# Performance work log

Measured on AMD Instinct MI355X. Metric: run time of the kernel, lower is better.

Reference implementation:

```python
import jax, jax.numpy as jnp
import numpy as np

NP, P, NS = 5, 5, 15  # body parts, joints per part, segments per scale


def _gauss_forward(x):
    # x: (batch, nb_frames, joints=NP*P, coordinates, 1)
    b, T, J, C, _ = x.shape
    inp = x.reshape(b, T, NP, P, C, 1)
    # lengths of the 6 temporal windows: full, two halves, three thirds
    seg_lens = [T, T // 2, T - T // 2, T // 3, T // 3, T - 2 * (T // 3)]
    outs = []
    for L in seg_lens:
        nb_fr = L // NS
        # first NS-1 segments of nb_fr frames each, always starting at frame 0
        head = inp[:, :(NS - 1) * nb_fr].reshape(b, NS - 1, nb_fr, NP, P, C, 1)
        mu_h = head.mean(axis=2)                    # (b, NS-1, NP, P, C, 1)
        xc = head - mu_h[:, :, None]
        cov_h = jnp.einsum('bkfnpci,bkfnpdi->bknpcd', xc, xc) / nb_fr
        # last segment runs to the END of the full sequence (faithful to original)
        tail = inp[:, (NS - 1) * nb_fr:]
        rest = tail.shape[1]
        mu_t = tail.mean(axis=1)                    # (b, NP, P, C, 1)
        xt = tail - mu_t[:, None]
        cov_t = jnp.einsum('bfnpci,bfnpdi->bnpcd', xt, xt) / rest
        mu = jnp.concatenate([mu_h, mu_t[:, None]], axis=1)    # (b, NS, NP, P, C, 1)
        cov = jnp.concatenate([cov_h, cov_t[:, None]], axis=1)  # (b, NS, NP, P, C, C)
        # match torch layout (b, NP, NS, P, ...)
        mu = jnp.transpose(mu, (0, 2, 1, 3, 4, 5))
        cov = jnp.transpose(cov, (0, 2, 1, 3, 4, 5))
        muT = jnp.swapaxes(mu, -1, -2)
        elt00 = cov + mu @ muT                       # E[xx^T]
        ones = jnp.ones(mu.shape[:-2] + (1, 1), dtype=x.dtype)
        top = jnp.concatenate([elt00, mu], axis=-1)
        bot = jnp.concatenate([muT, ones], axis=-1)
        outs.append(jnp.concatenate([top, bot], axis=-2))
    # (b, 6, NP, NS, P, C+1, C+1)
    return jnp.stack(outs, axis=1)


def setup_inputs() -> dict:
    key = jax.random.key(0)
    x = jax.random.normal(key, (256, 2048, 25, 3, 1), dtype=jnp.float32)
    return {"x": x}


def reference(x):
    return _gauss_forward(x)
```

## Files before the change

### kernel.cpp

```cpp
#include <hip/hip_runtime.h>
#include <stdint.h>


#define NSEG_MAX 40
#define IDXPK 0x9210287517640543ull

struct Tab {
    int n;
    uint32_t p[NSEG_MAX];
    uint32_t cr[45];
};

__global__ __launch_bounds__(256) void p1_kernel(const float* __restrict__ x,
                                                 float* __restrict__ ws, Tab tab) {
    __shared__ float lds[2250];
    int pc = blockIdx.x, b = blockIdx.y;
    uint32_t pk = tab.p[pc];
    int f0 = pk & 0xffff, L = (int)(pk >> 16);
    int tid = threadIdx.x;

    float s0=0.f,s1=0.f,s2=0.f,s3=0.f,s4=0.f,s5=0.f,s6=0.f,s7=0.f,s8=0.f;
    if (tid < 250) {
        int fslot = tid / 25;
        const float* q = x + (size_t)b * 153600 + (size_t)f0 * 75 + tid * 3;
        int nk = (L - fslot + 9) / 10;
        #pragma unroll 3
        for (int k = 0; k < nk; ++k, q += 750) {
            float a = q[0], bb = q[1], c = q[2];
            s0 += a;      s1 += bb;     s2 += c;
            s3 += a * a;  s4 += a * bb; s5 += a * c;
            s6 += bb * bb; s7 += bb * c; s8 += c * c;
        }
        float* l = &lds[tid * 9];
        l[0]=s0; l[1]=s1; l[2]=s2; l[3]=s3; l[4]=s4; l[5]=s5; l[6]=s6; l[7]=s7; l[8]=s8;
    }
    __syncthreads();
    if (tid < 225) {
        float v = 0.f;
        #pragma unroll
        for (int fs = 0; fs < 10; ++fs) v += lds[fs * 225 + tid];
        ws[((size_t)b * tab.n + pc) * 225 + tid] = v;
    }
}

__global__ __launch_bounds__(256) void p2_kernel(const float* __restrict__ ws,
                                                 float* __restrict__ out, Tab tab) {
    __shared__ float sws[1620];
    __shared__ float red[2032];
    __shared__ float invn[45];
    int b = blockIdx.x, np = blockIdx.y;
    int tid = threadIdx.x;
    int n = tab.n;
    int tot = n * 45;
    const float* wb = ws + (size_t)b * n * 225 + np * 45;
    for (int i = tid; i < tot; i += 256) {
        int piece = i / 45, idx = i - piece * 45;
        sws[i] = wb[(size_t)piece * 225 + idx];
    }
    if (tid < 45) {
        int st = tid / 15, ch = tid - st * 15;
        const int nst[3] = {136, 68, 45};
        int ns = nst[st];
        int nfr = (ch == 14) ? (2048 - 14 * ns) : ns;
        invn[tid] = 1.0f / (float)nfr;
    }
    __syncthreads();

    for (int i = tid; i < 2025; i += 256) {
        int sc = i / 45, idx = i - sc * 45;
        uint32_t r = tab.cr[sc];
        int p0 = (int)(r & 0xffff), p1 = (int)(r >> 16);
        float v = 0.f;
        for (int p = p0; p < p1; ++p) v += sws[p * 45 + idx];
        red[i] = v;
    }
    __syncthreads();

    float4* ob4 = (float4*)(out + (size_t)b * 36000 + (size_t)np * 1200);
    for (int q = tid; q < 1800; q += 256) {
        int seg = q / 300;
        int q2  = q - seg * 300;
        int ch  = q2 / 20;
        int rem = q2 - ch * 20;
        int p   = rem >> 2;
        int r   = rem & 3;
        int st  = (seg == 0) ? 0 : (seg < 3) ? 1 : 2;
        int sc  = st * 15 + ch;
        float inv = invn[sc];
        const float* rb = &red[sc * 45 + p * 9];
        uint64_t pkk = IDXPK >> (16 * r);
        float4 v;
        v.x = rb[(int)(pkk & 15)] * inv;
        v.y = rb[(int)((pkk >> 4) & 15)] * inv;
        v.z = rb[(int)((pkk >> 8) & 15)] * inv;
        v.w = (r == 3) ? 1.0f : rb[(int)((pkk >> 12) & 15)] * inv;
        ob4[(size_t)seg * 1500 + q2] = v;
    }
}

__global__ __launch_bounds__(256) void gauss_fallback(const float* __restrict__ x,
                                                      float* __restrict__ out) {
    __shared__ float lds[2250];
    __shared__ float red[225];
    __shared__ float outm[400];
    int bid = blockIdx.x;
    int chunk = bid % 15;
    int tmp = bid / 15;
    int stype = tmp % 3;
    int b = tmp / 3;
    const int nbs[3] = {136, 68, 45};
    int ns = nbs[stype];
    int f0 = chunk * ns;
    int f1 = (chunk == 14) ? 2048 : (f0 + ns);
    float inv_n = 1.0f / (float)(f1 - f0);
    int tid = threadIdx.x;
    if (tid < 250) {
        int j = tid % 25, tsub = tid / 25;
        const float* base = x + (size_t)b * 153600 + j * 3;
        float s0=0.f,s1=0.f,s2=0.f,s3=0.f,s4=0.f,s5=0.f,s6=0.f,s7=0.f,s8=0.f;
        for (int t = f0 + tsub; t < f1; t += 10) {
            const float* p = base + (size_t)t * 75;
            float x0 = p[0], x1 = p[1], x2 = p[2];
            s0+=x0; s1+=x1; s2+=x2;
            s3+=x0*x0; s4+=x0*x1; s5+=x0*x2;
            s6+=x1*x1; s7+=x1*x2; s8+=x2*x2;
        }
        float* l = &lds[tid * 9];
        l[0]=s0; l[1]=s1; l[2]=s2; l[3]=s3; l[4]=s4; l[5]=s5; l[6]=s6; l[7]=s7; l[8]=s8;
    }
    __syncthreads();
    if (tid < 225) {
        float v = 0.f;
        #pragma unroll
        for (int ts = 0; ts < 10; ++ts) v += lds[ts * 225 + tid];
        red[tid] = v;
    }
    __syncthreads();
    if (tid < 25) {
        const float* r = &red[tid * 9];
        float mu0=r[0]*inv_n, mu1=r[1]*inv_n, mu2=r[2]*inv_n;
        float m00=r[3]*inv_n, m01=r[4]*inv_n, m02=r[5]*inv_n;
        float m11=r[6]*inv_n, m12=r[7]*inv_n, m22=r[8]*inv_n;
        float* o = &outm[tid * 16];
        o[0]=m00; o[1]=m01; o[2]=m02; o[3]=mu0;
        o[4]=m01; o[5]=m11; o[6]=m12; o[7]=mu1;
        o[8]=m02; o[9]=m12; o[10]=m22; o[11]=mu2;
        o[12]=mu0; o[13]=mu1; o[14]=mu2; o[15]=1.0f;
    }
    __syncthreads();
    int so0 = (stype == 0) ? 0 : (stype == 1) ? 1 : 3;
    int ndup = (stype == 0) ? 1 : (stype == 1) ? 2 : 3;
    int total = 400 * ndup;
    size_t obase = (size_t)b * 36000 + (size_t)chunk * 80;
    for (int idx = tid; idx < total; idx += 256) {
        int dup = idx / 400;
        int r = idx % 400;
        int np = r / 80;
        int rem = r % 80;
        out[obase + (size_t)(so0 + dup) * 6000 + (size_t)np * 1200 + rem] = outm[r];
    }
}

static void build_tab(Tab& tab) {
    unsigned char isb[2049];
    for (int i = 0; i <= 2048; ++i) isb[i] = 0;
    isb[2048] = 1;
    for (int k = 1; k <= 14; ++k) { isb[45 * k] = 1; isb[68 * k] = 1; isb[136 * k] = 1; }
    int n = 0, prev = 0;
    int pf0[NSEG_MAX];
    for (int f = 1; f <= 2048; ++f) {
        if (!isb[f]) continue;
        pf0[n] = prev;
        tab.p[n++] = (uint32_t)(prev | ((f - prev) << 16));
        prev = f;
    }
    tab.n = n;
    const int nst[3] = {136, 68, 45};
    for (int st = 0; st < 3; ++st) {
        int ns = nst[st];
        for (int c = 0; c < 15; ++c) {
            int a = c * ns, bnd = (c == 14) ? 2048 : (c + 1) * ns;
            int p0 = 0; while (p0 < n && pf0[p0] < a) ++p0;
            int p1 = p0; while (p1 < n && pf0[p1] < bnd) ++p1;
            tab.cr[st * 15 + c] = (uint32_t)(p0 | (p1 << 16));
        }
    }
}

extern "C" void kernel_launch(void* const* d_in, const int* in_sizes, int n_in,
                              void* d_out, int out_size, void* d_ws, size_t ws_size,
                              hipStream_t stream) {
    const float* x = (const float*)d_in[0];
    float* out = (float*)d_out;
    Tab tab;
    build_tab(tab);
    size_t need = (size_t)256 * tab.n * 225 * sizeof(float);

    if (ws_size >= need) {
        float* ws = (float*)d_ws;
        dim3 g1(tab.n, 256);
        p1_kernel<<<g1, 256, 0, stream>>>(x, ws, tab);
        dim3 g2(256, 5);
        p2_kernel<<<g2, 256, 0, stream>>>(ws, out, tab);
    } else {
        gauss_fallback<<<256 * 45, 256, 0, stream>>>(x, out);
    }
}
```

Before: 239.5 us.

## Fuse piece reduction and output assembly into one kernel via last-block counter

Merges the two kernels into one. Each block writes its partial sums, then bumps a per-batch atomic counter, and the last block to finish for a batch performs the second-stage reduction and output writes for all five body parts. This removes the second kernel launch and the gap between kernels, but needs a memset for the counters and serialises the tail work of each batch into a single block. The first loop's unroll factor also goes from 3 to 5.

```diff
diff --git a/kernel.cpp b/kernel.cpp
--- a/kernel.cpp
+++ b/kernel.cpp
@@ -11,52 +11,54 @@
     uint32_t cr[45];
 };
 
-__global__ __launch_bounds__(256) void p1_kernel(const float* __restrict__ x,
-                                                 float* __restrict__ ws, Tab tab) {
-    __shared__ float lds[2250];
+__global__ __launch_bounds__(256) void fused_kernel(const float* __restrict__ x,
+                                                    float* __restrict__ ws,
+                                                    unsigned* __restrict__ cnt,
+                                                    float* __restrict__ out, Tab tab) {
+    __shared__ float smem[3870];
+    __shared__ int lastFlag;
     int pc = blockIdx.x, b = blockIdx.y;
+    int n = tab.n;
     uint32_t pk = tab.p[pc];
     int f0 = pk & 0xffff, L = (int)(pk >> 16);
     int tid = threadIdx.x;
 
-    float s0=0.f,s1=0.f,s2=0.f,s3=0.f,s4=0.f,s5=0.f,s6=0.f,s7=0.f,s8=0.f;
     if (tid < 250) {
         int fslot = tid / 25;
         const float* q = x + (size_t)b * 153600 + (size_t)f0 * 75 + tid * 3;
         int nk = (L - fslot + 9) / 10;
-        #pragma unroll 3
+        float s0=0.f,s1=0.f,s2=0.f,s3=0.f,s4=0.f,s5=0.f,s6=0.f,s7=0.f,s8=0.f;
+        #pragma unroll 5
         for (int k = 0; k < nk; ++k, q += 750) {
             float a = q[0], bb = q[1], c = q[2];
-            s0 += a;      s1 += bb;     s2 += c;
-            s3 += a * a;  s4 += a * bb; s5 += a * c;
-            s6 += bb * bb; s7 += bb * c; s8 += c * c;
-        }
-        float* l = &lds[tid * 9];
+            s0 += a;       s1 += bb;      s2 += c;
+            s3 += a * a;   s4 += a * bb;  s5 += a * c;
+            s6 += bb * bb; s7 += bb * c;  s8 += c * c;
+        }
+        float* l = &smem[tid * 9];
         l[0]=s0; l[1]=s1; l[2]=s2; l[3]=s3; l[4]=s4; l[5]=s5; l[6]=s6; l[7]=s7; l[8]=s8;
     }
     __syncthreads();
     if (tid < 225) {
         float v = 0.f;
         #pragma unroll
-        for (int fs = 0; fs < 10; ++fs) v += lds[fs * 225 + tid];
-        ws[((size_t)b * tab.n + pc) * 225 + tid] = v;
-    }
-}
-
-__global__ __launch_bounds__(256) void p2_kernel(const float* __restrict__ ws,
-                                                 float* __restrict__ out, Tab tab) {
-    __shared__ float sws[1620];
-    __shared__ float red[2032];
-    __shared__ float invn[45];
-    int b = blockIdx.x, np = blockIdx.y;
-    int tid = threadIdx.x;
-    int n = tab.n;
-    int tot = n * 45;
-    const float* wb = ws + (size_t)b * n * 225 + np * 45;
-    for (int i = tid; i < tot; i += 256) {
-        int piece = i / 45, idx = i - piece * 45;
-        sws[i] = wb[(size_t)piece * 225 + idx];
-    }
+        for (int fs = 0; fs < 10; ++fs) v += smem[fs * 225 + tid];
+        ws[((size_t)b * n + pc) * 225 + tid] = v;
+    }
+    __syncthreads();
+
+    if (tid == 0) {
+        __threadfence();
+        unsigned old = atomicAdd(&cnt[b], 1u);
+        lastFlag = (old == (unsigned)(n - 1));
+    }
+    __syncthreads();
+    if (!lastFlag) return;
+    __threadfence();
+
+    float* sws  = smem;
+    float* red  = smem + 1800;
+    float* invn = smem + 3825;
     if (tid < 45) {
         int st = tid / 15, ch = tid - st * 15;
         const int nst[3] = {136, 68, 45};
@@ -64,37 +66,45 @@
         int nfr = (ch == 14) ? (2048 - 14 * ns) : ns;
         invn[tid] = 1.0f / (float)nfr;
     }
-    __syncthreads();
-
-    for (int i = tid; i < 2025; i += 256) {
-        int sc = i / 45, idx = i - sc * 45;
-        uint32_t r = tab.cr[sc];
-        int p0 = (int)(r & 0xffff), p1 = (int)(r >> 16);
-        float v = 0.f;
-        for (int p = p0; p < p1; ++p) v += sws[p * 45 + idx];
-        red[i] = v;
-    }
-    __syncthreads();
-
-    float4* ob4 = (float4*)(out + (size_t)b * 36000 + (size_t)np * 1200);
-    for (int q = tid; q < 1800; q += 256) {
-        int seg = q / 300;
-        int q2  = q - seg * 300;
-        int ch  = q2 / 20;
-        int rem = q2 - ch * 20;
-        int p   = rem >> 2;
-        int r   = rem & 3;
-        int st  = (seg == 0) ? 0 : (seg < 3) ? 1 : 2;
-        int sc  = st * 15 + ch;
-        float inv = invn[sc];
-        const float* rb = &red[sc * 45 + p * 9];
-        uint64_t pkk = IDXPK >> (16 * r);
-        float4 v;
-        v.x = rb[(int)(pkk & 15)] * inv;
-        v.y = rb[(int)((pkk >> 4) & 15)] * inv;
-        v.z = rb[(int)((pkk >> 8) & 15)] * inv;
-        v.w = (r == 3) ? 1.0f : rb[(int)((pkk >> 12) & 15)] * inv;
-        ob4[(size_t)seg * 1500 + q2] = v;
+    const float* wbase = ws + (size_t)b * n * 225;
+    float4* ob4b = (float4*)(out + (size_t)b * 36000);
+    int tot = n * 45;
+    for (int np = 0; np < 5; ++np) {
+        for (int i = tid; i < tot; i += 256) {
+            int piece = i / 45, idx = i - piece * 45;
+            sws[i] = wbase[(size_t)piece * 225 + np * 45 + idx];
+        }
+        __syncthreads();
+        for (int i = tid; i < 2025; i += 256) {
+            int sc = i / 45, idx = i - sc * 45;
+            uint32_t r = tab.cr[sc];
+            int p0 = (int)(r & 0xffff), p1 = (int)(r >> 16);
+            float v = 0.f;
+            for (int p = p0; p < p1; ++p) v += sws[p * 45 + idx];
+            red[i] = v;
+        }
+        __syncthreads();
+        float4* ob4 = ob4b + (size_t)np * 300;
+        for (int q = tid; q < 1800; q += 256) {
+            int seg = q / 300;
+            int q2  = q - seg * 300;
+            int ch  = q2 / 20;
+            int rem = q2 - ch * 20;
+            int p   = rem >> 2;
+            int r   = rem & 3;
+            int st  = (seg == 0) ? 0 : (seg < 3) ? 1 : 2;
+            int sc  = st * 15 + ch;
+            float inv = invn[sc];
+            const float* rb = &red[sc * 45 + p * 9];
+            uint64_t pkk = IDXPK >> (16 * r);
+            float4 v;
+            v.x = rb[(int)(pkk & 15)] * inv;
+            v.y = rb[(int)((pkk >> 4) & 15)] * inv;
+            v.z = rb[(int)((pkk >> 8) & 15)] * inv;
+            v.w = (r == 3) ? 1.0f : rb[(int)((pkk >> 12) & 15)] * inv;
+            ob4[(size_t)seg * 1500 + q2] = v;
+        }
+        __syncthreads();
     }
 }
 
@@ -194,14 +204,15 @@
     float* out = (float*)d_out;
     Tab tab;
     build_tab(tab);
-    size_t need = (size_t)256 * tab.n * 225 * sizeof(float);
+    size_t ws_floats = (size_t)256 * tab.n * 225;
+    size_t need = ws_floats * sizeof(float) + 256 * sizeof(unsigned);
 
     if (ws_size >= need) {
         float* ws = (float*)d_ws;
-        dim3 g1(tab.n, 256);
-        p1_kernel<<<g1, 256, 0, stream>>>(x, ws, tab);
-        dim3 g2(256, 5);
-        p2_kernel<<<g2, 256, 0, stream>>>(ws, out, tab);
+        unsigned* cnt = (unsigned*)((char*)d_ws + ws_floats * sizeof(float));
+        hipMemsetAsync(cnt, 0, 256 * sizeof(unsigned), stream);
+        dim3 g(tab.n, 256);
+        fused_kernel<<<g, 256, 0, stream>>>(x, ws, cnt, out, tab);
     } else {
         gauss_fallback<<<256 * 45, 256, 0, stream>>>(x, out);
     }
```

After: 818.5 us. 242% more time.
